# Kernel optimization log

Hardware: AMD Instinct MI355X
Metric: run time of the kernel (lower is better)

Reference implementation:

```python
import jax, jax.numpy as jnp
import numpy as np

# NormControlledResidual config: control_mode='relative', norms_or_ratios=(1.0, 0.2)
# relative mode -> cumulative norms: [1.0, 1.0*0.2]
_NORMS = (1.0, 1.0 * 0.2)
_EPS = 1e-8

V, E, H, DS, S, L, B, NL = 1024, 512, 512, 1024, 128, 128, 512, 2


def _nc_residual(ctx_emb, hid_cat):
    a = ctx_emb / (jnp.linalg.norm(ctx_emb, axis=-1, keepdims=True) + _EPS) * _NORMS[0]
    b = hid_cat / (jnp.linalg.norm(hid_cat, axis=-1, keepdims=True) + _EPS) * _NORMS[1]
    return a + b


def setup_inputs() -> dict:
    key = jax.random.key(0)
    ks = jax.random.split(key, 12)
    scale = 0.05
    return {
        'sot_id': 0,
        'src_emb': jax.random.normal(ks[0], (S, B, E), jnp.float32),
        'src_outputs': jax.random.normal(ks[1], (S, B, DS), jnp.float32),
        'mask_src': jnp.ones((B, S), dtype=bool),
        'target': jax.random.randint(ks[2], (L, B), 0, V),
        'emb_W': jax.random.normal(ks[3], (V, E), jnp.float32) * scale,   # tied emb/proj
        'W_ih': jax.random.normal(ks[4], (NL, 4 * H, E), jnp.float32) * scale,
        'W_hh': jax.random.normal(ks[5], (NL, 4 * H, H), jnp.float32) * scale,
        'b_ih': jnp.zeros((NL, 4 * H), jnp.float32),
        'b_hh': jnp.zeros((NL, 4 * H), jnp.float32),
        'Wa': jax.random.normal(ks[6], (DS, H), jnp.float32) * scale,
        'W_h': jax.random.normal(ks[7], (H, DS + H), jnp.float32) * scale,
        'b_h': jnp.zeros((H,), jnp.float32),
    }


def reference(sot_id, src_emb, src_outputs, mask_src, target, emb_W,
              W_ih, W_hh, b_ih, b_hh, Wa, W_h, b_h):
    n_layers = W_ih.shape[0]
    bsz = target.shape[1]
    hdim = W_hh.shape[-1]
    # precompute attention keys once: [S, B, H]
    Wh_s = jnp.einsum('sbd,dt->sbt', src_outputs, Wa)
    neg = jnp.asarray(-1e9, src_outputs.dtype)
    # teacher-forced inputs: sot, target[0..L-2]
    inputs_seq = jnp.concatenate(
        [jnp.full((1, bsz), sot_id, dtype=target.dtype), target[:-1]], axis=0)
    h0 = jnp.zeros((n_layers, bsz, hdim), src_outputs.dtype)
    c0 = jnp.zeros_like(h0)

    def step(carry, inp):
        h, c = carry
        x = emb_W[inp]  # [B, E]
        new_h, new_c = [], []
        for l in range(n_layers):  # fixed small layer count
            gates = x @ W_ih[l].T + b_ih[l] + h[l] @ W_hh[l].T + b_hh[l]
            i, f, g, o = jnp.split(gates, 4, axis=-1)  # torch gate order i,f,g,o
            cl = jax.nn.sigmoid(f) * c[l] + jax.nn.sigmoid(i) * jnp.tanh(g)
            hl = jax.nn.sigmoid(o) * jnp.tanh(cl)
            new_h.append(hl)
            new_c.append(cl)
            x = hl
        hid_rnn = x  # top-layer hidden [B, H]
        scores = jnp.einsum('sbt,bt->bs', Wh_s, hid_rnn)
        scores = jnp.where(mask_src, scores, neg)
        almt = jax.nn.softmax(scores, axis=-1)                 # [B, S]
        ctx = jnp.einsum('bs,sbd->bd', almt, src_outputs)      # [B, DS]
        hid_cat = jnp.concatenate([hid_rnn, ctx], axis=-1) @ W_h.T + b_h
        ctx_emb = jnp.einsum('bs,sbe->be', almt, src_emb)      # [B, E]
        hid_res = _nc_residual(ctx_emb, hid_cat)
        logit = hid_res @ emb_W.T                              # tied projection
        log_prob = jax.nn.log_softmax(logit, axis=-1)
        return (jnp.stack(new_h), jnp.stack(new_c)), (log_prob, almt)

    _, (log_probs, almt_distrs) = jax.lax.scan(step, (h0, c0), inputs_seq)
    return log_probs, almt_distrs  # [L,B,V], [L,B,S]
```

## Files before the change

### kernel.cpp

```cpp
#include <hip/hip_runtime.h>
#include <cstddef>
#include <cstdint>


namespace {

typedef short  short8  __attribute__((ext_vector_type(8)));
typedef short  short4v __attribute__((ext_vector_type(4)));
typedef float  f32x4   __attribute__((ext_vector_type(4)));

constexpr int    kB  = 512;
constexpr int    kL  = 128;
constexpr int    kS  = 128;
constexpr int    kH  = 512;
constexpr int    kV  = 1024;
constexpr int    kG  = 2048;
constexpr int    kLB = kL * kB;
constexpr size_t kBH = (size_t)kB * kH;

__device__ __forceinline__ float sigmf(float x) { return 1.f / (1.f + expf(-x)); }

__device__ __forceinline__ unsigned short f2b(float f) {
    union { float f; unsigned u; } v; v.f = f;
    unsigned r = v.u + 0x7fffu + ((v.u >> 16) & 1u);
    return (unsigned short)(r >> 16);
}

__device__ __forceinline__ float b2f(unsigned short u) {
    union { unsigned u; float f; } v; v.u = (unsigned)u << 16;
    return v.f;
}

__device__ __forceinline__ f32x4 mfma16(short8 a, short8 b, f32x4 c) {
    return __builtin_amdgcn_mfma_f32_16x16x32_bf16(a, b, c, 0, 0, 0);
}

__global__ __launch_bounds__(256) void k_zero16(uint4* __restrict__ p, int n16) {
    int i = blockIdx.x * 256 + threadIdx.x;
    if (i < n16) p[i] = make_uint4(0u, 0u, 0u, 0u);
}

__global__ __launch_bounds__(256) void k_f2b(const float* __restrict__ in,
                                             unsigned short* __restrict__ o, int n) {
    int i = (blockIdx.x * 256 + threadIdx.x) * 4;
    if (i < n) {
        float4 v = *(const float4*)(in + i);
        short4v p; p[0] = (short)f2b(v.x); p[1] = (short)f2b(v.y);
        p[2] = (short)f2b(v.z); p[3] = (short)f2b(v.w);
        *(short4v*)(o + i) = p;
    }
}

__global__ __launch_bounds__(256) void k_waT(const float* __restrict__ Wa,
                                             unsigned short* __restrict__ WaT) {
    __shared__ float tile[32][33];
    const int d0 = blockIdx.x * 32, t0 = blockIdx.y * 32;
    const int r = threadIdx.x >> 3, c4 = (threadIdx.x & 7) * 4;
    const float4 v = *(const float4*)(Wa + (size_t)(d0 + r) * 512 + t0 + c4);
    tile[r][c4] = v.x; tile[r][c4 + 1] = v.y; tile[r][c4 + 2] = v.z; tile[r][c4 + 3] = v.w;
    __syncthreads();
    short4v o;
    o[0] = (short)f2b(tile[c4 + 0][r]); o[1] = (short)f2b(tile[c4 + 1][r]);
    o[2] = (short)f2b(tile[c4 + 2][r]); o[3] = (short)f2b(tile[c4 + 3][r]);
    *(short4v*)(WaT + (size_t)(t0 + r) * 1024 + d0 + c4) = o;
}

__global__ __launch_bounds__(256) void k_bsum(const float* __restrict__ a,
                                              const float* __restrict__ b,
                                              float* __restrict__ o) {
    int i = blockIdx.x * 256 + threadIdx.x;
    if (i < 2048) o[i] = a[i] + b[i];
}

template<int MODE>
__global__ __launch_bounds__(256) void k_mgemm(
    const void* __restrict__ Asrc1, const void* __restrict__ Asrc2,
    const unsigned short* __restrict__ Bw,
    const float* __restrict__ bias1, const float* __restrict__ bias2,
    const int* __restrict__ tgt, const int* __restrict__ sot,
    void* __restrict__ Cout)
{
    constexpr int KT = (MODE == 1) ? 1024 : ((MODE == 2) ? 1536 : 512);
    constexpr int CN = (MODE == 0) ? 2048 : ((MODE == 3) ? 1024 : 512);
    constexpr bool OUT_BF16 = (MODE == 0 || MODE == 1);

    __shared__ unsigned short Asm[128 * 40];
    __shared__ unsigned short Bsm[128 * 40];

    const int tid = threadIdx.x;
    const int m0 = blockIdx.x * 128, n0 = blockIdx.y * 128;
    const int srow = tid >> 1;
    const int kc   = (tid & 1) * 16;

    const unsigned short* ap1 = nullptr;
    const unsigned short* ap2 = nullptr;
    const float* ap1f = nullptr;
    if constexpr (MODE == 0) {
        const int m = m0 + srow;
        const int arow = (m < kB) ? sot[0] : tgt[m - kB];
        ap1 = (const unsigned short*)Asrc1 + (size_t)arow * 512;
    } else if constexpr (MODE == 1) {
        ap1f = (const float*)Asrc1 + (size_t)(m0 + srow) * 1024;
    } else if constexpr (MODE == 2) {
        ap1 = (const unsigned short*)Asrc1 + (size_t)(m0 + srow) * 512;
        ap2 = (const unsigned short*)Asrc2 + (size_t)(m0 + srow) * 1024;
    } else {
        ap1 = (const unsigned short*)Asrc1 + (size_t)(m0 + srow) * 512;
    }
    const unsigned short* bp = Bw + (size_t)(n0 + srow) * KT;

    f32x4 acc[4][4];
    #pragma unroll
    for (int i = 0; i < 4; ++i)
        #pragma unroll
        for (int j = 0; j < 4; ++j)
            #pragma unroll
            for (int r = 0; r < 4; ++r) acc[i][j][r] = 0.f;

    const int wid = tid >> 6, lane = tid & 63;
    const int wr = wid >> 1, wc = wid & 1;
    const int l16 = lane & 15, q8 = lane >> 4;

    for (int k0 = 0; k0 < KT; k0 += 32) {
        short8 av0, av1;
        if constexpr (MODE == 1) {
            const float* p = ap1f + k0 + kc;
            const float4 f0 = *(const float4*)(p);
            const float4 f1 = *(const float4*)(p + 4);
            const float4 f2 = *(const float4*)(p + 8);
            const float4 f3 = *(const float4*)(p + 12);
            av0[0] = (short)f2b(f0.x); av0[1] = (short)f2b(f0.y);
            av0[2] = (short)f2b(f0.z); av0[3] = (short)f2b(f0.w);
            av0[4] = (short)f2b(f1.x); av0[5] = (short)f2b(f1.y);
            av0[6] = (short)f2b(f1.z); av0[7] = (short)f2b(f1.w);
            av1[0] = (short)f2b(f2.x); av1[1] = (short)f2b(f2.y);
            av1[2] = (short)f2b(f2.z); av1[3] = (short)f2b(f2.w);
            av1[4] = (short)f2b(f3.x); av1[5] = (short)f2b(f3.y);
            av1[6] = (short)f2b(f3.z); av1[7] = (short)f2b(f3.w);
        } else if constexpr (MODE == 2) {
            const unsigned short* p = (k0 < 512) ? (ap1 + k0) : (ap2 + (k0 - 512));
            av0 = *(const short8*)(p + kc);
            av1 = *(const short8*)(p + kc + 8);
        } else {
            av0 = *(const short8*)(ap1 + k0 + kc);
            av1 = *(const short8*)(ap1 + k0 + kc + 8);
        }
        const short8 bv0 = *(const short8*)(bp + k0 + kc);
        const short8 bv1 = *(const short8*)(bp + k0 + kc + 8);
        *(short8*)&Asm[srow * 40 + kc]     = av0;
        *(short8*)&Asm[srow * 40 + kc + 8] = av1;
        *(short8*)&Bsm[srow * 40 + kc]     = bv0;
        *(short8*)&Bsm[srow * 40 + kc + 8] = bv1;
        __syncthreads();
        short8 af[4], bf[4];
        #pragma unroll
        for (int i = 0; i < 4; ++i)
            af[i] = *(const short8*)&Asm[(wr * 64 + i * 16 + l16) * 40 + q8 * 8];
        #pragma unroll
        for (int j = 0; j < 4; ++j)
            bf[j] = *(const short8*)&Bsm[(wc * 64 + j * 16 + l16) * 40 + q8 * 8];
        #pragma unroll
        for (int i = 0; i < 4; ++i)
            #pragma unroll
            for (int j = 0; j < 4; ++j)
                acc[i][j] = mfma16(af[i], bf[j], acc[i][j]);
        __syncthreads();
    }

    const int orow = m0 + wr * 64 + q8 * 4;
    const int ocol = n0 + wc * 64 + l16;
    #pragma unroll
    for (int j = 0; j < 4; ++j) {
        const int col = ocol + j * 16;
        float badd = 0.f;
        if constexpr (MODE == 0) badd = bias1[col] + bias2[col];
        if constexpr (MODE == 2) badd = bias1[col];
        #pragma unroll
        for (int i = 0; i < 4; ++i) {
            const int row = orow + i * 16;
            #pragma unroll
            for (int r = 0; r < 4; ++r) {
                const float v = acc[i][j][r] + badd;
                if constexpr (OUT_BF16)
                    ((unsigned short*)Cout)[(size_t)(row + r) * CN + col] = f2b(v);
                else
                    ((float*)Cout)[(size_t)(row + r) * CN + col] = v;
            }
        }
    }
}

__global__ __launch_bounds__(256) void k_step(
    const unsigned short* __restrict__ Whh0,
    const unsigned short* __restrict__ Wih1,
    const unsigned short* __restrict__ Whh1,
    const unsigned short* __restrict__ G0t,
    const float* __restrict__ bsum1,
    float* __restrict__ c0, float* __restrict__ c1,
    const unsigned short* __restrict__ h0r, unsigned short* __restrict__ h0w,
    const unsigned short* __restrict__ h1r, unsigned short* __restrict__ h1w,
    unsigned short* __restrict__ h1all_out,
    int ph)
{
    const int tid = threadIdx.x;
    const int g = tid >> 6, lane = tid & 63;
    const int l16 = lane & 15, q8 = lane >> 4;
    const int bx = blockIdx.x;
    const int kk = bx >> 3;
    const int ji = (bx & 7) * 2 + (kk & 1);
    const int bi = kk >> 1;
    const int b0 = bi * 32, j0 = ji * 32;
    const int bl = tid >> 3, j4 = (tid & 7) * 4;
    const int brow = b0 + bl;

    __shared__ float gl0[4][32][36];
    __shared__ float gl1[4][32][36];

    float giA[4], gfA[4], ggA[4], goA[4], c0A[4], c1A[4], bA[4][4];
    if (ph < kL) {
        const unsigned short* g0p = G0t + (size_t)brow * (size_t)kG + j0 + j4;
        const short4v a = *(const short4v*)(g0p);
        const short4v b = *(const short4v*)(g0p + 512);
        const short4v c = *(const short4v*)(g0p + 1024);
        const short4v d = *(const short4v*)(g0p + 1536);
        #pragma unroll
        for (int q = 0; q < 4; ++q) {
            giA[q] = b2f((unsigned short)a[q]);
            gfA[q] = b2f((unsigned short)b[q]);
            ggA[q] = b2f((unsigned short)c[q]);
            goA[q] = b2f((unsigned short)d[q]);
        }
        const float4 cv = *(const float4*)(c0 + (size_t)brow * 512 + j0 + j4);
        c0A[0]=cv.x; c0A[1]=cv.y; c0A[2]=cv.z; c0A[3]=cv.w;
    }
    if (ph >= 1) {
        const float4 cv = *(const float4*)(c1 + (size_t)brow * 512 + j0 + j4);
        c1A[0]=cv.x; c1A[1]=cv.y; c1A[2]=cv.z; c1A[3]=cv.w;
        #pragma unroll
        for (int gi = 0; gi < 4; ++gi) {
            const float4 bv = *(const float4*)(bsum1 + gi * 512 + j0 + j4);
            bA[gi][0]=bv.x; bA[gi][1]=bv.y; bA[gi][2]=bv.z; bA[gi][3]=bv.w;
        }
    }

    f32x4 acc0[2][2];
    #pragma unroll
    for (int i = 0; i < 2; ++i)
        #pragma unroll
        for (int j = 0; j < 2; ++j)
            #pragma unroll
            for (int r = 0; r < 4; ++r) acc0[i][j][r] = 0.f;
    if (ph < kL) {
        const unsigned short* a0p = h0r + (size_t)(b0 + l16) * 512 + q8 * 8;
        const unsigned short* w0p = Whh0 + (size_t)(g * 512 + j0 + l16) * 512 + q8 * 8;
        #pragma unroll
        for (int kq = 0; kq < 16; ++kq) {
            const short8 a0 = *(const short8*)(a0p + kq * 32);
            const short8 a1 = *(const short8*)(a0p + 16 * 512 + kq * 32);
            const short8 w0 = *(const short8*)(w0p + kq * 32);
            const short8 w1 = *(const short8*)(w0p + 16 * 512 + kq * 32);
            acc0[0][0] = mfma16(a0, w0, acc0[0][0]);
            acc0[0][1] = mfma16(a0, w1, acc0[0][1]);
            acc0[1][0] = mfma16(a1, w0, acc0[1][0]);
            acc0[1][1] = mfma16(a1, w1, acc0[1][1]);
        }
    }

    f32x4 acc1[2][2];
    #pragma unroll
    for (int i = 0; i < 2; ++i)
        #pragma unroll
        for (int j = 0; j < 2; ++j)
            #pragma unroll
            for (int r = 0; r < 4; ++r) acc1[i][j][r] = 0.f;
    if (ph >= 1) {
        const unsigned short* x0 = h0r + (size_t)(b0 + l16) * 512 + q8 * 8;
        const unsigned short* wi1 = Wih1 + (size_t)(g * 512 + j0 + l16) * 512 + q8 * 8;
        #pragma unroll
        for (int kq = 0; kq < 16; ++kq) {
            const short8 a0 = *(const short8*)(x0 + kq * 32);
            const short8 a1 = *(const short8*)(x0 + 16 * 512 + kq * 32);
            const short8 w0 = *(const short8*)(wi1 + kq * 32);
            const short8 w1 = *(const short8*)(wi1 + 16 * 512 + kq * 32);
            acc1[0][0] = mfma16(a0, w0, acc1[0][0]);
            acc1[0][1] = mfma16(a0, w1, acc1[0][1]);
            acc1[1][0] = mfma16(a1, w0, acc1[1][0]);
            acc1[1][1] = mfma16(a1, w1, acc1[1][1]);
        }
        const unsigned short* h1rp = h1r + (size_t)(b0 + l16) * 512 + q8 * 8;
        const unsigned short* wh1 = Whh1 + (size_t)(g * 512 + j0 + l16) * 512 + q8 * 8;
        #pragma unroll
        for (int kq = 0; kq < 16; ++kq) {
            const short8 a0 = *(const short8*)(h1rp + kq * 32);
            const short8 a1 = *(const short8*)(h1rp + 16 * 512 + kq * 32);
            const short8 w0 = *(const short8*)(wh1 + kq * 32);
            const short8 w1 = *(const short8*)(wh1 + 16 * 512 + kq * 32);
            acc1[0][0] = mfma16(a0, w0, acc1[0][0]);
            acc1[0][1] = mfma16(a0, w1, acc1[0][1]);
            acc1[1][0] = mfma16(a1, w0, acc1[1][0]);
            acc1[1][1] = mfma16(a1, w1, acc1[1][1]);
        }
    }

    if (ph < kL) {
        #pragma unroll
        for (int i = 0; i < 2; ++i)
            #pragma unroll
            for (int j = 0; j < 2; ++j)
                #pragma unroll
                for (int r = 0; r < 4; ++r)
                    gl0[g][i * 16 + q8 * 4 + r][j * 16 + l16] = acc0[i][j][r];
    }
    if (ph >= 1) {
        #pragma unroll
        for (int i = 0; i < 2; ++i)
            #pragma unroll
            for (int j = 0; j < 2; ++j)
                #pragma unroll
                for (int r = 0; r < 4; ++r)
                    gl1[g][i * 16 + q8 * 4 + r][j * 16 + l16] = acc1[i][j][r];
    }
    __syncthreads();

    if (ph < kL) {
        float4 cn; float* cnp = (float*)&cn;
        short4v hb;
        #pragma unroll
        for (int q = 0; q < 4; ++q) {
            const float iv = gl0[0][bl][j4 + q] + giA[q];
            const float fv = gl0[1][bl][j4 + q] + gfA[q];
            const float gv = gl0[2][bl][j4 + q] + ggA[q];
            const float ov = gl0[3][bl][j4 + q] + goA[q];
            const float cc = sigmf(fv) * c0A[q] + sigmf(iv) * tanhf(gv);
            const float hh = sigmf(ov) * tanhf(cc);
            cnp[q] = cc; hb[q] = (short)f2b(hh);
        }
        *(float4*)(c0 + (size_t)brow * 512 + j0 + j4) = cn;
        *(short4v*)(h0w + (size_t)brow * 512 + j0 + j4) = hb;
    }
    if (ph >= 1) {
        float4 cn; float* cnp = (float*)&cn;
        short4v hb;
        #pragma unroll
        for (int q = 0; q < 4; ++q) {
            const float iv = gl1[0][bl][j4 + q] + bA[0][q];
            const float fv = gl1[1][bl][j4 + q] + bA[1][q];
            const float gv = gl1[2][bl][j4 + q] + bA[2][q];
            const float ov = gl1[3][bl][j4 + q] + bA[3][q];
            const float cc = sigmf(fv) * c1A[q] + sigmf(iv) * tanhf(gv);
            const float hh = sigmf(ov) * tanhf(cc);
            cnp[q] = cc; hb[q] = (short)f2b(hh);
        }
        *(float4*)(c1 + (size_t)brow * 512 + j0 + j4) = cn;
        *(short4v*)(h1w + (size_t)brow * 512 + j0 + j4) = hb;
        *(short4v*)(h1all_out + (size_t)brow * 512 + j0 + j4) = hb;
    }
}

__global__ __launch_bounds__(256) void k_scores(
    const unsigned short* __restrict__ h1all, const unsigned short* __restrict__ whs,
    float* __restrict__ almt)
{
    const int b = blockIdx.x;
    const int tid = threadIdx.x;
    const int wid = tid >> 6, lane = tid & 63;
    const int wr = wid >> 1, wc = wid & 1;
    const int l16 = lane & 15, q8 = lane >> 4;

    f32x4 acc[4][4];
    #pragma unroll
    for (int i = 0; i < 4; ++i)
        #pragma unroll
        for (int j = 0; j < 4; ++j)
            #pragma unroll
            for (int r = 0; r < 4; ++r) acc[i][j][r] = 0.f;

    const unsigned short* Ab = h1all + (size_t)b * 512;
    const unsigned short* Bb = whs   + (size_t)b * 512;
    for (int k0 = 0; k0 < 512; k0 += 32) {
        short8 af[4], bfr[4];
        #pragma unroll
        for (int i = 0; i < 4; ++i)
            af[i] = *(const short8*)(Ab + (size_t)(wr * 64 + i * 16 + l16) * kBH + k0 + q8 * 8);
        #pragma unroll
        for (int j = 0; j < 4; ++j)
            bfr[j] = *(const short8*)(Bb + (size_t)(wc * 64 + j * 16 + l16) * kBH + k0 + q8 * 8);
        #pragma unroll
        for (int i = 0; i < 4; ++i)
            #pragma unroll
            for (int j = 0; j < 4; ++j)
                acc[i][j] = mfma16(af[i], bfr[j], acc[i][j]);
    }

    __shared__ float sm[128][132];
    #pragma unroll
    for (int i = 0; i < 4; ++i)
        #pragma unroll
        for (int j = 0; j < 4; ++j)
            #pragma unroll
            for (int r = 0; r < 4; ++r)
                sm[wr * 64 + i * 16 + q8 * 4 + r][wc * 64 + j * 16 + l16] = acc[i][j][r];
    __syncthreads();

    const int row = tid >> 1, half = tid & 1;
    const float* sr = &sm[row][half * 64];
    float mx = -1e30f;
    for (int cc = 0; cc < 64; ++cc) mx = fmaxf(mx, sr[cc]);
    mx = fmaxf(mx, __shfl_xor(mx, 1));
    float s = 0.f;
    for (int cc = 0; cc < 64; ++cc) s += expf(sr[cc] - mx);
    s += __shfl_xor(s, 1);
    const float inv = 1.f / s;
    float* dst = almt + ((size_t)row * kB + b) * kS + half * 64;
    for (int c4 = 0; c4 < 16; ++c4) {
        float4 o;
        o.x = expf(sr[c4 * 4 + 0] - mx) * inv;
        o.y = expf(sr[c4 * 4 + 1] - mx) * inv;
        o.z = expf(sr[c4 * 4 + 2] - mx) * inv;
        o.w = expf(sr[c4 * 4 + 3] - mx) * inv;
        *(float4*)(dst + c4 * 4) = o;
    }
}

__global__ __launch_bounds__(256) void k_srcT(
    const float* __restrict__ so, const float* __restrict__ se,
    unsigned short* __restrict__ srcT)
{
    const int b = blockIdx.x;
    const int dt = blockIdx.y;
    const float* src; int fdim, d0, dbase;
    if (dt < 8) { src = so; fdim = 1024; d0 = dt * 128;       dbase = d0; }
    else        { src = se; fdim = 512;  d0 = (dt - 8) * 128; dbase = 1024 + d0; }

    __shared__ unsigned short tl[128][136];
    const int tid = threadIdx.x;
    {
        const int srow = tid >> 1, cc = (tid & 1) * 64;
        const float* p = src + ((size_t)srow * kB + b) * fdim + d0 + cc;
        unsigned short* dd = &tl[srow][cc];
        #pragma unroll
        for (int q = 0; q < 16; ++q) {
            const float4 v = *(const float4*)(p + q * 4);
            dd[q * 4 + 0] = f2b(v.x); dd[q * 4 + 1] = f2b(v.y);
            dd[q * 4 + 2] = f2b(v.z); dd[q * 4 + 3] = f2b(v.w);
        }
    }
    __syncthreads();
    {
        const int drow = tid >> 1, s0 = (tid & 1) * 64;
        unsigned short* o = srcT + ((size_t)b * 1536 + dbase + drow) * 128 + s0;
        #pragma unroll
        for (int q = 0; q < 8; ++q) {
            short8 v;
            #pragma unroll
            for (int r = 0; r < 8; ++r) v[r] = (short)tl[s0 + q * 8 + r][drow];
            *(short8*)(o + q * 8) = v;
        }
    }
}

__global__ __launch_bounds__(256) void k_ctxm(
    const float* __restrict__ almt, const unsigned short* __restrict__ srcT,
    unsigned short* __restrict__ ctxb, float* __restrict__ ctxemb)
{
    const int b = blockIdx.x;
    const int tid = threadIdx.x;
    const int wid = tid >> 6, lane = tid & 63;
    const int wt = wid >> 1, wd = wid & 1;
    const int l16 = lane & 15, q8 = lane >> 4;

    short8 af[4][4];
    #pragma unroll
    for (int i = 0; i < 4; ++i) {
        const float* p = almt + ((size_t)(wt * 64 + i * 16 + l16) * kB + b) * kS + q8 * 8;
        #pragma unroll
        for (int kq = 0; kq < 4; ++kq) {
            const float4 v0 = *(const float4*)(p + kq * 32);
            const float4 v1 = *(const float4*)(p + kq * 32 + 4);
            short8 t;
            t[0] = (short)f2b(v0.x); t[1] = (short)f2b(v0.y);
            t[2] = (short)f2b(v0.z); t[3] = (short)f2b(v0.w);
            t[4] = (short)f2b(v1.x); t[5] = (short)f2b(v1.y);
            t[6] = (short)f2b(v1.z); t[7] = (short)f2b(v1.w);
            af[i][kq] = t;
        }
    }

    const unsigned short* sb = srcT + (size_t)b * 1536 * 128;
    #pragma unroll 1
    for (int dt = 0; dt < 24; ++dt) {
        const int d0 = dt * 64 + wd * 32;
        f32x4 acc[4][2];
        #pragma unroll
        for (int i = 0; i < 4; ++i)
            #pragma unroll
            for (int j = 0; j < 2; ++j)
                #pragma unroll
                for (int r = 0; r < 4; ++r) acc[i][j][r] = 0.f;
        #pragma unroll
        for (int kq = 0; kq < 4; ++kq) {
            const short8 bf0 = *(const short8*)(sb + (size_t)(d0 + l16) * 128 + kq * 32 + q8 * 8);
            const short8 bf1 = *(const short8*)(sb + (size_t)(d0 + 16 + l16) * 128 + kq * 32 + q8 * 8);
            #pragma unroll
            for (int i = 0; i < 4; ++i) {
                acc[i][0] = mfma16(af[i][kq], bf0, acc[i][0]);
                acc[i][1] = mfma16(af[i][kq], bf1, acc[i][1]);
            }
        }
        if (dt < 16) {
            #pragma unroll
            for (int i = 0; i < 4; ++i)
                #pragma unroll
                for (int j = 0; j < 2; ++j) {
                    const int d = d0 + j * 16 + l16;
                    #pragma unroll
                    for (int r = 0; r < 4; ++r) {
                        const int tr = wt * 64 + i * 16 + q8 * 4 + r;
                        ctxb[((size_t)tr * kB + b) * 1024 + d] = f2b(acc[i][j][r]);
                    }
                }
        } else {
            #pragma unroll
            for (int i = 0; i < 4; ++i)
                #pragma unroll
                for (int j = 0; j < 2; ++j) {
                    const int d = d0 + j * 16 + l16 - 1024;
                    #pragma unroll
                    for (int r = 0; r < 4; ++r) {
                        const int tr = wt * 64 + i * 16 + q8 * 4 + r;
                        ctxemb[((size_t)tr * kB + b) * 512 + d] = acc[i][j][r];
                    }
                }
        }
    }
}

__global__ __launch_bounds__(256) void k_ncres(
    const float* __restrict__ ctxemb, const float* __restrict__ hc,
    unsigned short* __restrict__ res)
{
    const int row  = blockIdx.x * 4 + (threadIdx.x >> 6);
    const int lane = threadIdx.x & 63;
    const float* ce = ctxemb + (size_t)row * 512 + lane * 8;
    const float* hp = hc + (size_t)row * 512 + lane * 8;
    const float4 c0v = *(const float4*)(ce);
    const float4 c1v = *(const float4*)(ce + 4);
    const float4 h0v = *(const float4*)(hp);
    const float4 h1v = *(const float4*)(hp + 4);
    float sc = c0v.x*c0v.x + c0v.y*c0v.y + c0v.z*c0v.z + c0v.w*c0v.w
             + c1v.x*c1v.x + c1v.y*c1v.y + c1v.z*c1v.z + c1v.w*c1v.w;
    float sh = h0v.x*h0v.x + h0v.y*h0v.y + h0v.z*h0v.z + h0v.w*h0v.w
             + h1v.x*h1v.x + h1v.y*h1v.y + h1v.z*h1v.z + h1v.w*h1v.w;
    for (int m = 1; m < 64; m <<= 1) { sc += __shfl_xor(sc, m); sh += __shfl_xor(sh, m); }
    const float rc = 1.0f / (sqrtf(sc) + 1e-8f);
    const float rh = 0.2f / (sqrtf(sh) + 1e-8f);
    short8 o;
    o[0] = (short)f2b(c0v.x * rc + h0v.x * rh);
    o[1] = (short)f2b(c0v.y * rc + h0v.y * rh);
    o[2] = (short)f2b(c0v.z * rc + h0v.z * rh);
    o[3] = (short)f2b(c0v.w * rc + h0v.w * rh);
    o[4] = (short)f2b(c1v.x * rc + h1v.x * rh);
    o[5] = (short)f2b(c1v.y * rc + h1v.y * rh);
    o[6] = (short)f2b(c1v.z * rc + h1v.z * rh);
    o[7] = (short)f2b(c1v.w * rc + h1v.w * rh);
    *(short8*)(res + (size_t)row * 512 + lane * 8) = o;
}

__global__ __launch_bounds__(256) void k_lsm(float* __restrict__ out)
{
    const int row  = blockIdx.x * 4 + (threadIdx.x >> 6);
    const int lane = threadIdx.x & 63;
    float* p = out + (size_t)row * 1024 + lane * 16;
    float4 v[4];
    #pragma unroll
    for (int q = 0; q < 4; ++q) v[q] = *(const float4*)(p + q * 4);
    float mx = v[0].x;
    #pragma unroll
    for (int q = 0; q < 4; ++q)
        mx = fmaxf(mx, fmaxf(fmaxf(v[q].x, v[q].y), fmaxf(v[q].z, v[q].w)));
    for (int m = 1; m < 64; m <<= 1) mx = fmaxf(mx, __shfl_xor(mx, m));
    float sm = 0.f;
    #pragma unroll
    for (int q = 0; q < 4; ++q)
        sm += expf(v[q].x - mx) + expf(v[q].y - mx) + expf(v[q].z - mx) + expf(v[q].w - mx);
    for (int m = 1; m < 64; m <<= 1) sm += __shfl_xor(sm, m);
    const float lse = mx + logf(sm);
    #pragma unroll
    for (int q = 0; q < 4; ++q)
        *(float4*)(p + q * 4) = make_float4(v[q].x - lse, v[q].y - lse, v[q].z - lse, v[q].w - lse);
}

}

extern "C" void kernel_launch(void* const* d_in, const int* in_sizes, int n_in,
                              void* d_out, int out_size, void* d_ws, size_t ws_size,
                              hipStream_t stream)
{
    const int*   sot     = (const int*)d_in[0];
    const float* src_emb = (const float*)d_in[1];
    const float* src_out = (const float*)d_in[2];
    const int*   target  = (const int*)d_in[4];
    const float* embW    = (const float*)d_in[5];
    const float* Wih     = (const float*)d_in[6];
    const float* Whh     = (const float*)d_in[7];
    const float* bih     = (const float*)d_in[8];
    const float* bhh     = (const float*)d_in[9];
    const float* Wa      = (const float*)d_in[10];
    const float* Wh      = (const float*)d_in[11];
    const float* bhv     = (const float*)d_in[12];

    float* out_lp   = (float*)d_out;
    float* out_almt = out_lp + (size_t)kLB * kV;

    uint8_t* w = (uint8_t*)d_ws;
    unsigned short* G0b    = (unsigned short*)w;
    unsigned short* srcT   = (unsigned short*)w;
    unsigned short* ctx_b  = (unsigned short*)(w + 201326592ull);
    float* ctxemb          = (float*)(w + 335544320ull);
    float* hidcat          = (float*)(w + 0ull);
    unsigned short* hidres = (unsigned short*)(w + 134217728ull);
    unsigned short* whs_b  = (unsigned short*)(w + 536870912ull);
    unsigned short* h1all_b= (unsigned short*)(w + 603979776ull);
    uint8_t* wcv = w + 671088640ull;
    unsigned short* embW_b = (unsigned short*)wcv;
    unsigned short* WihB   = (unsigned short*)(wcv + 1048576ull);
    unsigned short* WhhB   = (unsigned short*)(wcv + 5242880ull);
    unsigned short* WaT    = (unsigned short*)(wcv + 9437184ull);
    unsigned short* WhB    = (unsigned short*)(wcv + 10485760ull);
    float* bsum1           = (float*)(wcv + 12058624ull);
    uint8_t* st = wcv + 12066816ull;
    float* c0p             = (float*)st;
    float* c1p             = (float*)(st + 1048576ull);
    unsigned short* h0p    = (unsigned short*)(st + 2097152ull);
    unsigned short* h1p    = (unsigned short*)(st + 3145728ull);

    k_zero16<<<dim3(1024), dim3(256), 0, stream>>>((uint4*)st, 262144);

    k_f2b<<<dim3(512),  dim3(256), 0, stream>>>(embW, embW_b, 524288);
    k_f2b<<<dim3(2048), dim3(256), 0, stream>>>(Wih,  WihB,   2097152);
    k_f2b<<<dim3(2048), dim3(256), 0, stream>>>(Whh,  WhhB,   2097152);
    k_f2b<<<dim3(768),  dim3(256), 0, stream>>>(Wh,   WhB,    786432);
    k_waT<<<dim3(32, 16), dim3(256), 0, stream>>>(Wa, WaT);
    k_bsum<<<dim3(8), dim3(256), 0, stream>>>(bih + 2048, bhh + 2048, bsum1);

    k_mgemm<0><<<dim3(512, 16), dim3(256), 0, stream>>>(
        embW_b, nullptr, WihB, bih, bhh, target, sot, G0b);
    k_mgemm<1><<<dim3(512, 4), dim3(256), 0, stream>>>(
        src_out, nullptr, WaT, nullptr, nullptr, nullptr, nullptr, whs_b);

    for (int ph = 0; ph <= kL; ++ph) {
        k_step<<<dim3(256), dim3(256), 0, stream>>>(
            WhhB, WihB + (size_t)kG * kH, WhhB + (size_t)kG * kH,
            G0b + (size_t)(ph < kL ? ph : 0) * kB * kG, bsum1,
            c0p, c1p,
            h0p + (size_t)(ph & 1) * kBH, h0p + (size_t)((ph + 1) & 1) * kBH,
            h1p + (size_t)((ph & 1) ^ 1) * kBH, h1p + (size_t)(ph & 1) * kBH,
            h1all_b + (size_t)(ph >= 1 ? ph - 1 : 0) * kBH, ph);
    }

    k_scores<<<dim3(512), dim3(256), 0, stream>>>(h1all_b, whs_b, out_almt);
    k_srcT<<<dim3(512, 12), dim3(256), 0, stream>>>(src_out, src_emb, srcT);
    k_ctxm<<<dim3(512), dim3(256), 0, stream>>>(out_almt, srcT, ctx_b, ctxemb);
    k_mgemm<2><<<dim3(512, 4), dim3(256), 0, stream>>>(
        h1all_b, ctx_b, WhB, bhv, nullptr, nullptr, nullptr, hidcat);
    k_ncres<<<dim3(16384), dim3(256), 0, stream>>>(ctxemb, hidcat, hidres);
    k_mgemm<3><<<dim3(512, 8), dim3(256), 0, stream>>>(
        hidres, nullptr, embW_b, nullptr, nullptr, nullptr, nullptr, out_lp);
    k_lsm<<<dim3(16384), dim3(256), 0, stream>>>(out_lp);

    (void)in_sizes; (void)n_in; (void)out_size; (void)ws_size;
}
```

Baseline: 5.133 ms.

## Precompute layer-0 input gates per vocab token and split-K the recurrent step

The input-gate GEMM for layer 0 no longer runs over every (timestep, batch) row. It now runs once over the 1024-entry embedding vocabulary, producing a small gate table. Each step kernel gathers its row from that table by token id, which removes a large GEMM and a big intermediate buffer write and read. The step kernel also goes from 256 to 512 threads and splits the K dimension across two wave groups, reducing the results through shared memory. This shortens the serial per-step latency, at the cost of more shared memory and an extra reduction.

```diff
diff --git a/kernel.cpp b/kernel.cpp
--- a/kernel.cpp
+++ b/kernel.cpp
@@ -77,12 +77,11 @@
     const void* __restrict__ Asrc1, const void* __restrict__ Asrc2,
     const unsigned short* __restrict__ Bw,
     const float* __restrict__ bias1, const float* __restrict__ bias2,
-    const int* __restrict__ tgt, const int* __restrict__ sot,
     void* __restrict__ Cout)
 {
     constexpr int KT = (MODE == 1) ? 1024 : ((MODE == 2) ? 1536 : 512);
-    constexpr int CN = (MODE == 0) ? 2048 : ((MODE == 3) ? 1024 : 512);
-    constexpr bool OUT_BF16 = (MODE == 0 || MODE == 1);
+    constexpr int CN = (MODE == 4) ? 2048 : ((MODE == 3) ? 1024 : 512);
+    constexpr bool OUT_BF16 = (MODE == 1 || MODE == 4);
 
     __shared__ unsigned short Asm[128 * 40];
     __shared__ unsigned short Bsm[128 * 40];
@@ -95,11 +94,7 @@
     const unsigned short* ap1 = nullptr;
     const unsigned short* ap2 = nullptr;
     const float* ap1f = nullptr;
-    if constexpr (MODE == 0) {
-        const int m = m0 + srow;
-        const int arow = (m < kB) ? sot[0] : tgt[m - kB];
-        ap1 = (const unsigned short*)Asrc1 + (size_t)arow * 512;
-    } else if constexpr (MODE == 1) {
+    if constexpr (MODE == 1) {
         ap1f = (const float*)Asrc1 + (size_t)(m0 + srow) * 1024;
     } else if constexpr (MODE == 2) {
         ap1 = (const unsigned short*)Asrc1 + (size_t)(m0 + srow) * 512;
@@ -173,7 +168,7 @@
     for (int j = 0; j < 4; ++j) {
         const int col = ocol + j * 16;
         float badd = 0.f;
-        if constexpr (MODE == 0) badd = bias1[col] + bias2[col];
+        if constexpr (MODE == 4) badd = bias1[col] + bias2[col];
         if constexpr (MODE == 2) badd = bias1[col];
         #pragma unroll
         for (int i = 0; i < 4; ++i) {
@@ -190,11 +185,12 @@
     }
 }
 
-__global__ __launch_bounds__(256) void k_step(
+__global__ __launch_bounds__(512) void k_step(
     const unsigned short* __restrict__ Whh0,
     const unsigned short* __restrict__ Wih1,
     const unsigned short* __restrict__ Whh1,
-    const unsigned short* __restrict__ G0t,
+    const unsigned short* __restrict__ G0tab,
+    const int* __restrict__ tgt, const int* __restrict__ sot,
     const float* __restrict__ bsum1,
     float* __restrict__ c0, float* __restrict__ c1,
     const unsigned short* __restrict__ h0r, unsigned short* __restrict__ h0w,
@@ -203,43 +199,45 @@
     int ph)
 {
     const int tid = threadIdx.x;
-    const int g = tid >> 6, lane = tid & 63;
+    const int wid = tid >> 6;
+    const int g = wid & 3, kh = wid >> 2;
+    const int lane = tid & 63;
     const int l16 = lane & 15, q8 = lane >> 4;
     const int bx = blockIdx.x;
     const int kk = bx >> 3;
     const int ji = (bx & 7) * 2 + (kk & 1);
     const int bi = kk >> 1;
     const int b0 = bi * 32, j0 = ji * 32;
-    const int bl = tid >> 3, j4 = (tid & 7) * 4;
-    const int brow = b0 + bl;
-
-    __shared__ float gl0[4][32][36];
-    __shared__ float gl1[4][32][36];
-
-    float giA[4], gfA[4], ggA[4], goA[4], c0A[4], c1A[4], bA[4][4];
+    const int kbase = kh * 256;
+
+    __shared__ float gl0[2][4][32][36];
+    __shared__ float gl1[2][4][32][36];
+
+    const int erow = tid >> 4;
+    const int ec0  = (tid & 15) * 2;
+    const int brow = b0 + erow;
+
+    float giA[2], gfA[2], ggA[2], goA[2], c0A[2], c1A[2], bA[4][2];
     if (ph < kL) {
-        const unsigned short* g0p = G0t + (size_t)brow * (size_t)kG + j0 + j4;
-        const short4v a = *(const short4v*)(g0p);
-        const short4v b = *(const short4v*)(g0p + 512);
-        const short4v c = *(const short4v*)(g0p + 1024);
-        const short4v d = *(const short4v*)(g0p + 1536);
-        #pragma unroll
-        for (int q = 0; q < 4; ++q) {
-            giA[q] = b2f((unsigned short)a[q]);
-            gfA[q] = b2f((unsigned short)b[q]);
-            ggA[q] = b2f((unsigned short)c[q]);
-            goA[q] = b2f((unsigned short)d[q]);
-        }
-        const float4 cv = *(const float4*)(c0 + (size_t)brow * 512 + j0 + j4);
-        c0A[0]=cv.x; c0A[1]=cv.y; c0A[2]=cv.z; c0A[3]=cv.w;
+        const int token = (ph == 0) ? sot[0] : tgt[(ph - 1) * kB + brow];
+        const unsigned short* g0p = G0tab + (size_t)token * kG + j0 + ec0;
+        #pragma unroll
+        for (int e = 0; e < 2; ++e) {
+            giA[e] = b2f(g0p[e]);
+            gfA[e] = b2f(g0p[512 + e]);
+            ggA[e] = b2f(g0p[1024 + e]);
+            goA[e] = b2f(g0p[1536 + e]);
+        }
+        const float2 cv = *(const float2*)(c0 + (size_t)brow * 512 + j0 + ec0);
+        c0A[0] = cv.x; c0A[1] = cv.y;
     }
     if (ph >= 1) {
-        const float4 cv = *(const float4*)(c1 + (size_t)brow * 512 + j0 + j4);
-        c1A[0]=cv.x; c1A[1]=cv.y; c1A[2]=cv.z; c1A[3]=cv.w;
+        const float2 cv = *(const float2*)(c1 + (size_t)brow * 512 + j0 + ec0);
+        c1A[0] = cv.x; c1A[1] = cv.y;
         #pragma unroll
         for (int gi = 0; gi < 4; ++gi) {
-            const float4 bv = *(const float4*)(bsum1 + gi * 512 + j0 + j4);
-            bA[gi][0]=bv.x; bA[gi][1]=bv.y; bA[gi][2]=bv.z; bA[gi][3]=bv.w;
+            const float2 bv = *(const float2*)(bsum1 + gi * 512 + j0 + ec0);
+            bA[gi][0] = bv.x; bA[gi][1] = bv.y;
         }
     }
 
@@ -251,10 +249,10 @@
             #pragma unroll
             for (int r = 0; r < 4; ++r) acc0[i][j][r] = 0.f;
     if (ph < kL) {
-        const unsigned short* a0p = h0r + (size_t)(b0 + l16) * 512 + q8 * 8;
-        const unsigned short* w0p = Whh0 + (size_t)(g * 512 + j0 + l16) * 512 + q8 * 8;
-        #pragma unroll
-        for (int kq = 0; kq < 16; ++kq) {
+        const unsigned short* a0p = h0r + (size_t)(b0 + l16) * 512 + kbase + q8 * 8;
+        const unsigned short* w0p = Whh0 + (size_t)(g * 512 + j0 + l16) * 512 + kbase + q8 * 8;
+        #pragma unroll
+        for (int kq = 0; kq < 8; ++kq) {
             const short8 a0 = *(const short8*)(a0p + kq * 32);
             const short8 a1 = *(const short8*)(a0p + 16 * 512 + kq * 32);
             const short8 w0 = *(const short8*)(w0p + kq * 32);
@@ -274,10 +272,10 @@
             #pragma unroll
             for (int r = 0; r < 4; ++r) acc1[i][j][r] = 0.f;
     if (ph >= 1) {
-        const unsigned short* x0 = h0r + (size_t)(b0 + l16) * 512 + q8 * 8;
-        const unsigned short* wi1 = Wih1 + (size_t)(g * 512 + j0 + l16) * 512 + q8 * 8;
-        #pragma unroll
-        for (int kq = 0; kq < 16; ++kq) {
+        const unsigned short* x0 = h0r + (size_t)(b0 + l16) * 512 + kbase + q8 * 8;
+        const unsigned short* wi1 = Wih1 + (size_t)(g * 512 + j0 + l16) * 512 + kbase + q8 * 8;
+        #pragma unroll
+        for (int kq = 0; kq < 8; ++kq) {
             const short8 a0 = *(const short8*)(x0 + kq * 32);
             const short8 a1 = *(const short8*)(x0 + 16 * 512 + kq * 32);
             const short8 w0 = *(const short8*)(wi1 + kq * 32);
@@ -287,10 +285,10 @@
             acc1[1][0] = mfma16(a1, w0, acc1[1][0]);
             acc1[1][1] = mfma16(a1, w1, acc1[1][1]);
         }
-        const unsigned short* h1rp = h1r + (size_t)(b0 + l16) * 512 + q8 * 8;
-        const unsigned short* wh1 = Whh1 + (size_t)(g * 512 + j0 + l16) * 512 + q8 * 8;
-        #pragma unroll
-        for (int kq = 0; kq < 16; ++kq) {
+        const unsigned short* h1rp = h1r + (size_t)(b0 + l16) * 512 + kbase + q8 * 8;
+        const unsigned short* wh1 = Whh1 + (size_t)(g * 512 + j0 + l16) * 512 + kbase + q8 * 8;
+        #pragma unroll
+        for (int kq = 0; kq < 8; ++kq) {
             const short8 a0 = *(const short8*)(h1rp + kq * 32);
             const short8 a1 = *(const short8*)(h1rp + 16 * 512 + kq * 32);
             const short8 w0 = *(const short8*)(wh1 + kq * 32);
@@ -309,7 +307,7 @@
             for (int j = 0; j < 2; ++j)
                 #pragma unroll
                 for (int r = 0; r < 4; ++r)
-                    gl0[g][i * 16 + q8 * 4 + r][j * 16 + l16] = acc0[i][j][r];
+                    gl0[kh][g][i * 16 + q8 * 4 + r][j * 16 + l16] = acc0[i][j][r];
     }
     if (ph >= 1) {
         #pragma unroll
@@ -318,42 +316,44 @@
             for (int j = 0; j < 2; ++j)
                 #pragma unroll
                 for (int r = 0; r < 4; ++r)
-                    gl1[g][i * 16 + q8 * 4 + r][j * 16 + l16] = acc1[i][j][r];
+                    gl1[kh][g][i * 16 + q8 * 4 + r][j * 16 + l16] = acc1[i][j][r];
     }
     __syncthreads();
 
     if (ph < kL) {
-        float4 cn; float* cnp = (float*)&cn;
-        short4v hb;
-        #pragma unroll
-        for (int q = 0; q < 4; ++q) {
-            const float iv = gl0[0][bl][j4 + q] + giA[q];
-            const float fv = gl0[1][bl][j4 + q] + gfA[q];
-            const float gv = gl0[2][bl][j4 + q] + ggA[q];
-            const float ov = gl0[3][bl][j4 + q] + goA[q];
-            const float cc = sigmf(fv) * c0A[q] + sigmf(iv) * tanhf(gv);
+        float cn[2]; unsigned short hb[2];
+        #pragma unroll
+        for (int e = 0; e < 2; ++e) {
+            const int col = ec0 + e;
+            const float iv = gl0[0][0][erow][col] + gl0[1][0][erow][col] + giA[e];
+            const float fv = gl0[0][1][erow][col] + gl0[1][1][erow][col] + gfA[e];
+            const float gv = gl0[0][2][erow][col] + gl0[1][2][erow][col] + ggA[e];
+            const float ov = gl0[0][3][erow][col] + gl0[1][3][erow][col] + goA[e];
+            const float cc = sigmf(fv) * c0A[e] + sigmf(iv) * tanhf(gv);
             const float hh = sigmf(ov) * tanhf(cc);
-            cnp[q] = cc; hb[q] = (short)f2b(hh);
-        }
-        *(float4*)(c0 + (size_t)brow * 512 + j0 + j4) = cn;
-        *(short4v*)(h0w + (size_t)brow * 512 + j0 + j4) = hb;
+            cn[e] = cc; hb[e] = f2b(hh);
+        }
+        *(float2*)(c0 + (size_t)brow * 512 + j0 + ec0) = make_float2(cn[0], cn[1]);
+        *(unsigned*)(h0w + (size_t)brow * 512 + j0 + ec0) =
+            (unsigned)hb[0] | ((unsigned)hb[1] << 16);
     }
     if (ph >= 1) {
-        float4 cn; float* cnp = (float*)&cn;
-        short4v hb;
-        #pragma unroll
-        for (int q = 0; q < 4; ++q) {
-            const float iv = gl1[0][bl][j4 + q] + bA[0][q];
-            const float fv = gl1[1][bl][j4 + q] + bA[1][q];
-            const float gv = gl1[2][bl][j4 + q] + bA[2][q];
-            const float ov = gl1[3][bl][j4 + q] + bA[3][q];
-            const float cc = sigmf(fv) * c1A[q] + sigmf(iv) * tanhf(gv);
+        float cn[2]; unsigned short hb[2];
+        #pragma unroll
+        for (int e = 0; e < 2; ++e) {
+            const int col = ec0 + e;
+            const float iv = gl1[0][0][erow][col] + gl1[1][0][erow][col] + bA[0][e];
+            const float fv = gl1[0][1][erow][col] + gl1[1][1][erow][col] + bA[1][e];
+            const float gv = gl1[0][2][erow][col] + gl1[1][2][erow][col] + bA[2][e];
+            const float ov = gl1[0][3][erow][col] + gl1[1][3][erow][col] + bA[3][e];
+            const float cc = sigmf(fv) * c1A[e] + sigmf(iv) * tanhf(gv);
             const float hh = sigmf(ov) * tanhf(cc);
-            cnp[q] = cc; hb[q] = (short)f2b(hh);
-        }
-        *(float4*)(c1 + (size_t)brow * 512 + j0 + j4) = cn;
-        *(short4v*)(h1w + (size_t)brow * 512 + j0 + j4) = hb;
-        *(short4v*)(h1all_out + (size_t)brow * 512 + j0 + j4) = hb;
+            cn[e] = cc; hb[e] = f2b(hh);
+        }
+        const unsigned packed = (unsigned)hb[0] | ((unsigned)hb[1] << 16);
+        *(float2*)(c1 + (size_t)brow * 512 + j0 + ec0) = make_float2(cn[0], cn[1]);
+        *(unsigned*)(h1w + (size_t)brow * 512 + j0 + ec0) = packed;
+        *(unsigned*)(h1all_out + (size_t)brow * 512 + j0 + ec0) = packed;
     }
 }
 
@@ -613,7 +613,6 @@
     float* out_almt = out_lp + (size_t)kLB * kV;
 
     uint8_t* w = (uint8_t*)d_ws;
-    unsigned short* G0b    = (unsigned short*)w;
     unsigned short* srcT   = (unsigned short*)w;
     unsigned short* ctx_b  = (unsigned short*)(w + 201326592ull);
     float* ctxemb          = (float*)(w + 335544320ull);
@@ -633,6 +632,7 @@
     float* c1p             = (float*)(st + 1048576ull);
     unsigned short* h0p    = (unsigned short*)(st + 2097152ull);
     unsigned short* h1p    = (unsigned short*)(st + 3145728ull);
+    unsigned short* G0tab  = (unsigned short*)(st + 4194304ull);
 
     k_zero16<<<dim3(1024), dim3(256), 0, stream>>>((uint4*)st, 262144);
 
@@ -643,15 +643,15 @@
     k_waT<<<dim3(32, 16), dim3(256), 0, stream>>>(Wa, WaT);
     k_bsum<<<dim3(8), dim3(256), 0, stream>>>(bih + 2048, bhh + 2048, bsum1);
 
-    k_mgemm<0><<<dim3(512, 16), dim3(256), 0, stream>>>(
-        embW_b, nullptr, WihB, bih, bhh, target, sot, G0b);
+    k_mgemm<4><<<dim3(8, 16), dim3(256), 0, stream>>>(
+        embW_b, nullptr, WihB, bih, bhh, G0tab);
     k_mgemm<1><<<dim3(512, 4), dim3(256), 0, stream>>>(
-        src_out, nullptr, WaT, nullptr, nullptr, nullptr, nullptr, whs_b);
+        src_out, nullptr, WaT, nullptr, nullptr, whs_b);
 
     for (int ph = 0; ph <= kL; ++ph) {
-        k_step<<<dim3(256), dim3(256), 0, stream>>>(
+        k_step<<<dim3(256), dim3(512), 0, stream>>>(
             WhhB, WihB + (size_t)kG * kH, WhhB + (size_t)kG * kH,
-            G0b + (size_t)(ph < kL ? ph : 0) * kB * kG, bsum1,
+            G0tab, target, sot, bsum1,
             c0p, c1p,
             h0p + (size_t)(ph & 1) * kBH, h0p + (size_t)((ph + 1) & 1) * kBH,
             h1p + (size_t)((ph & 1) ^ 1) * kBH, h1p + (size_t)(ph & 1) * kBH,
@@ -662,10 +662,10 @@
     k_srcT<<<dim3(512, 12), dim3(256), 0, stream>>>(src_out, src_emb, srcT);
     k_ctxm<<<dim3(512), dim3(256), 0, stream>>>(out_almt, srcT, ctx_b, ctxemb);
     k_mgemm<2><<<dim3(512, 4), dim3(256), 0, stream>>>(
-        h1all_b, ctx_b, WhB, bhv, nullptr, nullptr, nullptr, hidcat);
+        h1all_b, ctx_b, WhB, bhv, nullptr, hidcat);
     k_ncres<<<dim3(16384), dim3(256), 0, stream>>>(ctxemb, hidcat, hidres);
     k_mgemm<3><<<dim3(512, 8), dim3(256), 0, stream>>>(
-        hidres, nullptr, embW_b, nullptr, nullptr, nullptr, nullptr, out_lp);
+        hidres, nullptr, embW_b, nullptr, nullptr, out_lp);
     k_lsm<<<dim3(16384), dim3(256), 0, stream>>>(out_lp);
 
     (void)in_sizes; (void)n_in; (void)out_size; (void)ws_size;
```

New measurement: 4.631 ms. -9.8%, faster.
